# Optimization experiments

Hardware: AMD Instinct MI355X
Metric: run time of the kernel (lower is better)

The kernel has to match this reference:

```python
import jax, jax.numpy as jnp
import numpy as np

NEG_BIG = -9.0e15  # matches torch's -9000000000000000.0 mask fill
ALPHA = 0.2        # leakyrelu negative slope


def setup_inputs() -> dict:
    key = jax.random.key(0)
    k1, k2, k3, k4, k5 = jax.random.split(key, 5)
    N, F_in, F_out = 4096, 512, 64
    stdv = 1.0 / np.sqrt(F_out)
    x = jax.random.normal(k1, (N, F_in), dtype=jnp.float32)
    adj = jax.random.randint(k2, (N, N), 0, 2, dtype=jnp.int32)
    W = jax.random.uniform(k3, (F_in, F_out), dtype=jnp.float32, minval=-stdv, maxval=stdv)
    a = jax.random.normal(k4, (2 * F_out, 1), dtype=jnp.float32) * 0.1
    bias = jax.random.uniform(k5, (F_out,), dtype=jnp.float32, minval=-stdv, maxval=stdv)
    return {"x": x, "adj": adj, "W": W, "a": a, "bias": bias}


def _gat_forward(x, adj, W, a, bias):
    N = x.shape[0]
    F_out = W.shape[1]
    h = x @ W  # (N, F)
    a1 = a[:F_out, 0]   # weights hitting the first concat half
    a2 = a[F_out:, 0]   # weights hitting the second concat half
    # First half: row k=i*N+j of the concat holds h_j  ->  e1[j] = h_j . a1
    e1 = h @ a1  # (N,)
    # Second half of this repo's concat is NOT h_i; exact index algebra:
    # second[k=i*N+j, r] = h[(r*N+i)//F, (((r*N+i)%F)*N + j) % F]
    # Since it depends on j only via j % F, build table T[i, t] (t = j % F).
    r = jnp.arange(F_out)[:, None]          # (F, 1)
    i = jnp.arange(N)[None, :]              # (1, N)
    m = r * N + i                           # (F, N)
    p = m // F_out                          # row index into h
    s0 = m % F_out
    t = jnp.arange(F_out)                   # (F,)
    col = (s0[..., None] * N + t) % F_out   # (F, N, F) column index into h
    vals = h[p[..., None], col]             # (F, N, F)
    T = jnp.einsum('r,rit->it', a2, vals)   # (N, F)
    j = jnp.arange(N)
    e2 = T[:, j % F_out]                    # (N, N) second-half contribution
    e = e1[None, :] + e2                    # (N, N) pre-activation scores
    e = jnp.where(e > 0, e, ALPHA * e)      # LeakyReLU(0.2)
    e = jnp.where(adj > 0, e, NEG_BIG)      # mask non-edges
    att = jax.nn.softmax(e, axis=1)         # row-wise softmax (dropout = eval identity)
    out = jax.nn.relu(att @ h) + bias       # relu BEFORE bias add, as in source
    return out


def reference(x, adj, W, a, bias):
    return _gat_forward(x, adj, W, a, bias)
```

## Files before the change

kernel.cpp:

```cpp
#include <hip/hip_runtime.h>
#include <math.h>

#define N_NODES 4096
#define F_IN    512
#define F_OUT   64
#define ALPHA   0.2f
#define NPART   32

typedef _Float16 half8 __attribute__((ext_vector_type(8)));
typedef _Float16 half4 __attribute__((ext_vector_type(4)));
typedef float    floatx4 __attribute__((ext_vector_type(4)));

__global__ __launch_bounds__(256) void k_prep(const float* __restrict__ W,
                                              _Float16* __restrict__ WT) {
    int idx = blockIdx.x * 256 + threadIdx.x;
    int t = idx >> 9;
    int k = idx & 511;
    WT[idx] = (_Float16)W[k * F_OUT + t];
}

__global__ __launch_bounds__(256) void k_hW(const float* __restrict__ x,
                                            const _Float16* __restrict__ WT,
                                            const float* __restrict__ a,
                                            float* __restrict__ h,
                                            _Float16* __restrict__ hT,
                                            float* __restrict__ e1) {
    __shared__ float red[4][16][64];
    int tid  = threadIdx.x;
    int lane = tid & 63;
    int w    = tid >> 6;
    int i0   = blockIdx.x * 16;
    int n    = lane & 15;
    int quad = lane >> 4;

    floatx4 acc[4] = {{0,0,0,0},{0,0,0,0},{0,0,0,0},{0,0,0,0}};

    const float* xr = x + (size_t)(i0 + n) * F_IN + w * 128 + quad * 8;
    const _Float16* wb = WT + w * 128 + quad * 8;
#pragma unroll
    for (int kk = 0; kk < 128; kk += 32) {
        float4 x0 = *(const float4*)(xr + kk);
        float4 x1 = *(const float4*)(xr + kk + 4);
        half8 af = {(_Float16)x0.x, (_Float16)x0.y, (_Float16)x0.z, (_Float16)x0.w,
                    (_Float16)x1.x, (_Float16)x1.y, (_Float16)x1.z, (_Float16)x1.w};
#pragma unroll
        for (int g = 0; g < 4; ++g) {
            half8 bf = *(const half8*)(wb + (size_t)(g * 16 + n) * F_IN + kk);
            acc[g] = __builtin_amdgcn_mfma_f32_16x16x32_f16(af, bf, acc[g], 0, 0, 0);
        }
    }
#pragma unroll
    for (int g = 0; g < 4; ++g)
#pragma unroll
        for (int r = 0; r < 4; ++r)
            red[w][g * 4 + r][lane] = acc[g][r];
    __syncthreads();
    if (w != 0) return;
#pragma unroll
    for (int g = 0; g < 4; ++g)
#pragma unroll
        for (int r = 0; r < 4; ++r)
            acc[g][r] = red[0][g * 4 + r][lane] + red[1][g * 4 + r][lane] +
                        red[2][g * 4 + r][lane] + red[3][g * 4 + r][lane];
#pragma unroll
    for (int g = 0; g < 4; ++g) {
        half4 hv;
#pragma unroll
        for (int r = 0; r < 4; ++r) {
            h[(size_t)(i0 + quad * 4 + r) * F_OUT + g * 16 + n] = acc[g][r];
            hv[r] = (_Float16)acc[g][r];
        }
        *(half4*)(hT + (size_t)(g * 16 + n) * N_NODES + i0 + quad * 4) = hv;
    }
    float a1v[4];
#pragma unroll
    for (int g = 0; g < 4; ++g) a1v[g] = a[g * 16 + n];
#pragma unroll
    for (int r = 0; r < 4; ++r) {
        float v = acc[0][r] * a1v[0] + acc[1][r] * a1v[1] + acc[2][r] * a1v[2] + acc[3][r] * a1v[3];
        v += __shfl_xor(v, 1, 64);
        v += __shfl_xor(v, 2, 64);
        v += __shfl_xor(v, 4, 64);
        v += __shfl_xor(v, 8, 64);
        if (n == 0) e1[i0 + quad * 4 + r] = v;
    }
}

__global__ __launch_bounds__(256) void k_TqP(const float* __restrict__ h,
                                             const float* __restrict__ a,
                                             const float* __restrict__ e1,
                                             _Float16* __restrict__ P) {
    __shared__ float part[4][64];
    __shared__ float TqS[64];
    int q = blockIdx.x;
    int tid = threadIdx.x;
    int t = tid & 63;
    int rp = tid >> 6;
    const float* a2 = a + F_OUT;
    float s = 0.f;
#pragma unroll
    for (int rr = 0; rr < 16; ++rr) {
        int r = rp * 16 + rr;
        s += a2[r] * h[(size_t)(r * 64 + q) * F_OUT + t];
    }
    part[rp][t] = s;
    __syncthreads();
    if (tid < 64) TqS[tid] = part[0][tid] + part[1][tid] + part[2][tid] + part[3][tid];
    __syncthreads();
#pragma unroll
    for (int it = 0; it < 4; ++it) {
        int j = (it * 256 + tid) * 4;
        float4 ev = *(const float4*)(e1 + j);
        float4 tv = *(const float4*)(TqS + (j & 63));
        float e[4] = {ev.x + tv.x, ev.y + tv.y, ev.z + tv.z, ev.w + tv.w};
        half4 pv;
#pragma unroll
        for (int r = 0; r < 4; ++r) {
            float xx = e[r] > 0.f ? e[r] : ALPHA * e[r];
            pv[r] = (_Float16)__expf(xx);
        }
        *(half4*)(P + (size_t)q * N_NODES + j) = pv;
    }
}

__global__ __launch_bounds__(256, 4) void k_main(const int* __restrict__ adj,
                                                 const _Float16* __restrict__ P,
                                                 const _Float16* __restrict__ hT,
                                                 float* __restrict__ out_part,
                                                 float* __restrict__ den_part) {
    int tid  = threadIdx.x;
    int lane = tid & 63;
    int w    = tid >> 6;
    int b    = blockIdx.x;
    int s    = b & 31;
    int g    = (b >> 5) * 4 + w;
    int i0   = g * 16;
    int q    = i0 >> 6;
    int n    = lane & 15;
    int quad = lane >> 4;
    int jbase = s * 128 + quad * 8;

    const int*      arow = adj + (size_t)(i0 + n) * N_NODES + jbase;
    const _Float16* prow = P + (size_t)q * N_NODES + jbase;
    const _Float16* hrow = hT + (size_t)n * N_NODES + jbase;

    int4 a0[4], a1[4];
    half8 pv[4];
#pragma unroll
    for (int c = 0; c < 4; ++c) {
        a0[c] = *(const int4*)(arow + c * 32);
        a1[c] = *(const int4*)(arow + c * 32 + 4);
        pv[c] = *(const half8*)(prow + c * 32);
    }

    floatx4 acc[4] = {{0,0,0,0},{0,0,0,0},{0,0,0,0},{0,0,0,0}};
    floatx4 accd = {0, 0, 0, 0};
    _Float16 one_h = (n == 0) ? (_Float16)1.0f : (_Float16)0.0f;
    half8 ones_f = {one_h, one_h, one_h, one_h, one_h, one_h, one_h, one_h};

#pragma unroll
    for (int c = 0; c < 4; ++c) {
        int joff = c * 32;
        half8 af;
        af[0] = a0[c].x > 0 ? pv[c][0] : (_Float16)0.f;
        af[1] = a0[c].y > 0 ? pv[c][1] : (_Float16)0.f;
        af[2] = a0[c].z > 0 ? pv[c][2] : (_Float16)0.f;
        af[3] = a0[c].w > 0 ? pv[c][3] : (_Float16)0.f;
        af[4] = a1[c].x > 0 ? pv[c][4] : (_Float16)0.f;
        af[5] = a1[c].y > 0 ? pv[c][5] : (_Float16)0.f;
        af[6] = a1[c].z > 0 ? pv[c][6] : (_Float16)0.f;
        af[7] = a1[c].w > 0 ? pv[c][7] : (_Float16)0.f;
#pragma unroll
        for (int g4 = 0; g4 < 4; ++g4) {
            half8 bf = *(const half8*)(hrow + (size_t)g4 * 16 * N_NODES + joff);
            acc[g4] = __builtin_amdgcn_mfma_f32_16x16x32_f16(af, bf, acc[g4], 0, 0, 0);
        }
        accd = __builtin_amdgcn_mfma_f32_16x16x32_f16(af, ones_f, accd, 0, 0, 0);
    }
    float* op = out_part + ((size_t)s * N_NODES + i0) * F_OUT;
#pragma unroll
    for (int g4 = 0; g4 < 4; ++g4)
#pragma unroll
        for (int r = 0; r < 4; ++r)
            op[(quad * 4 + r) * F_OUT + g4 * 16 + n] = acc[g4][r];
    if (n == 0) {
#pragma unroll
        for (int r = 0; r < 4; ++r)
            den_part[s * N_NODES + i0 + quad * 4 + r] = accd[r];
    }
}

__global__ __launch_bounds__(256) void k_out(const float* __restrict__ out_part,
                                             const float* __restrict__ den_part,
                                             const float* __restrict__ bias,
                                             float* __restrict__ out) {
    int idx4 = blockIdx.x * 256 + threadIdx.x;
    int base = idx4 * 4;
    int i = base >> 6;
    int t = base & 63;
    float4 sacc = {0.f, 0.f, 0.f, 0.f};
    float dacc = 0.f;
#pragma unroll
    for (int p = 0; p < NPART; ++p) {
        float4 v = ((const float4*)(out_part + (size_t)p * N_NODES * F_OUT))[idx4];
        sacc.x += v.x; sacc.y += v.y; sacc.z += v.z; sacc.w += v.w;
        dacc += den_part[p * N_NODES + i];
    }
    float4 bv = *(const float4*)(bias + t);
    float4 o;
    o.x = fmaxf(sacc.x / dacc, 0.f) + bv.x;
    o.y = fmaxf(sacc.y / dacc, 0.f) + bv.y;
    o.z = fmaxf(sacc.z / dacc, 0.f) + bv.z;
    o.w = fmaxf(sacc.w / dacc, 0.f) + bv.w;
    ((float4*)out)[idx4] = o;
}

extern "C" void kernel_launch(void* const* d_in, const int* in_sizes, int n_in,
                              void* d_out, int out_size, void* d_ws, size_t ws_size,
                              hipStream_t stream) {
    const float* x    = (const float*)d_in[0];
    const int*   adj  = (const int*)d_in[1];
    const float* W    = (const float*)d_in[2];
    const float* a    = (const float*)d_in[3];
    const float* bias = (const float*)d_in[4];
    float* out = (float*)d_out;

    char* ws = (char*)d_ws;
    float*    h        = (float*)ws;
    _Float16* hT       = (_Float16*)(ws + 1024 * 1024);
    float*    e1       = (float*)(ws + 1536 * 1024);
    _Float16* P        = (_Float16*)(ws + 1552 * 1024);
    _Float16* WT       = (_Float16*)(ws + 2064 * 1024);
    float*    out_part = (float*)(ws + 2128 * 1024);
    float*    den_part = (float*)(ws + (2128 + 32768) * 1024);

    k_prep<<<128, 256, 0, stream>>>(W, WT);
    k_hW  <<<256, 256, 0, stream>>>(x, WT, a, h, hT, e1);
    k_TqP <<<64, 256, 0, stream>>>(h, a, e1, P);
    k_main<<<2048, 256, 0, stream>>>(adj, P, hT, out_part, den_part);
    k_out <<<256, 256, 0, stream>>>(out_part, den_part, bias, out);
}
```

Baseline: 139.7 us.

## Pack adjacency into bitmask and halve column partitions in main kernel

Adds a kernel that converts the int32 adjacency into a bitmask using wave ballots. The main attention kernel then reads 32-bit mask words and applies them with bitwise AND on the packed half probabilities. The number of column partitions drops from 32 to 16, so each block processes 256 columns, which halves the partial-output buffers and the reduction traffic. The full adjacency is still read once, now coalesced in the pack kernel, at the cost of an extra launch and a mask write.

```diff
diff --git a/kernel.cpp b/kernel.cpp
--- a/kernel.cpp
+++ b/kernel.cpp
@@ -5,11 +5,13 @@
 #define F_IN    512
 #define F_OUT   64
 #define ALPHA   0.2f
-#define NPART   32
+#define NPART   16
 
 typedef _Float16 half8 __attribute__((ext_vector_type(8)));
 typedef _Float16 half4 __attribute__((ext_vector_type(4)));
 typedef float    floatx4 __attribute__((ext_vector_type(4)));
+
+union H8U4 { half8 h; uint32_t u[4]; };
 
 __global__ __launch_bounds__(256) void k_prep(const float* __restrict__ W,
                                               _Float16* __restrict__ WT) {
@@ -17,6 +19,23 @@
     int t = idx >> 9;
     int k = idx & 511;
     WT[idx] = (_Float16)W[k * F_OUT + t];
+}
+
+__global__ __launch_bounds__(256) void k_pack(const int* __restrict__ adj,
+                                              unsigned long long* __restrict__ adjb) {
+    int tid  = threadIdx.x;
+    int lane = tid & 63;
+    int waveId = blockIdx.x * 4 + (tid >> 6);
+    int row  = waveId >> 1;
+    int half = waveId & 1;
+    const int* base = adj + (size_t)row * N_NODES + half * 2048 + lane;
+    unsigned long long* dst = adjb + row * 64 + half * 32;
+#pragma unroll 8
+    for (int c = 0; c < 32; ++c) {
+        int av = base[c * 64];
+        unsigned long long mk = __ballot(av > 0);
+        if (lane == 0) dst[c] = mk;
+    }
 }
 
 __global__ __launch_bounds__(256) void k_hW(const float* __restrict__ x,
@@ -123,7 +142,7 @@
     }
 }
 
-__global__ __launch_bounds__(256, 4) void k_main(const int* __restrict__ adj,
+__global__ __launch_bounds__(256, 4) void k_main(const unsigned int* __restrict__ adjb32,
                                                  const _Float16* __restrict__ P,
                                                  const _Float16* __restrict__ hT,
                                                  float* __restrict__ out_part,
@@ -132,26 +151,21 @@
     int lane = tid & 63;
     int w    = tid >> 6;
     int b    = blockIdx.x;
-    int s    = b & 31;
-    int g    = (b >> 5) * 4 + w;
+    int s    = b & 15;
+    int g    = (b >> 4) * 4 + w;
     int i0   = g * 16;
     int q    = i0 >> 6;
     int n    = lane & 15;
     int quad = lane >> 4;
-    int jbase = s * 128 + quad * 8;
-
-    const int*      arow = adj + (size_t)(i0 + n) * N_NODES + jbase;
+    int jbase = s * 256 + quad * 8;
+
+    const unsigned int* mrow = adjb32 + (size_t)(i0 + n) * (N_NODES / 32) + s * 8;
+    uint4 m0 = *(const uint4*)(mrow);
+    uint4 m1 = *(const uint4*)(mrow + 4);
+    unsigned int m32[8] = {m0.x, m0.y, m0.z, m0.w, m1.x, m1.y, m1.z, m1.w};
+
     const _Float16* prow = P + (size_t)q * N_NODES + jbase;
     const _Float16* hrow = hT + (size_t)n * N_NODES + jbase;
-
-    int4 a0[4], a1[4];
-    half8 pv[4];
-#pragma unroll
-    for (int c = 0; c < 4; ++c) {
-        a0[c] = *(const int4*)(arow + c * 32);
-        a1[c] = *(const int4*)(arow + c * 32 + 4);
-        pv[c] = *(const half8*)(prow + c * 32);
-    }
 
     floatx4 acc[4] = {{0,0,0,0},{0,0,0,0},{0,0,0,0},{0,0,0,0}};
     floatx4 accd = {0, 0, 0, 0};
@@ -159,23 +173,23 @@
     half8 ones_f = {one_h, one_h, one_h, one_h, one_h, one_h, one_h, one_h};
 
 #pragma unroll
-    for (int c = 0; c < 4; ++c) {
+    for (int c = 0; c < 8; ++c) {
         int joff = c * 32;
-        half8 af;
-        af[0] = a0[c].x > 0 ? pv[c][0] : (_Float16)0.f;
-        af[1] = a0[c].y > 0 ? pv[c][1] : (_Float16)0.f;
-        af[2] = a0[c].z > 0 ? pv[c][2] : (_Float16)0.f;
-        af[3] = a0[c].w > 0 ? pv[c][3] : (_Float16)0.f;
-        af[4] = a1[c].x > 0 ? pv[c][4] : (_Float16)0.f;
-        af[5] = a1[c].y > 0 ? pv[c][5] : (_Float16)0.f;
-        af[6] = a1[c].z > 0 ? pv[c][6] : (_Float16)0.f;
-        af[7] = a1[c].w > 0 ? pv[c][7] : (_Float16)0.f;
+        H8U4 pv, af;
+        pv.h = *(const half8*)(prow + joff);
+        unsigned int byte = (m32[c] >> (quad * 8)) & 0xFFu;
+#pragma unroll
+        for (int d = 0; d < 4; ++d) {
+            unsigned int msk = (((byte >> (2 * d)) & 1u) ? 0x0000FFFFu : 0u) |
+                               (((byte >> (2 * d + 1)) & 1u) ? 0xFFFF0000u : 0u);
+            af.u[d] = pv.u[d] & msk;
+        }
 #pragma unroll
         for (int g4 = 0; g4 < 4; ++g4) {
             half8 bf = *(const half8*)(hrow + (size_t)g4 * 16 * N_NODES + joff);
-            acc[g4] = __builtin_amdgcn_mfma_f32_16x16x32_f16(af, bf, acc[g4], 0, 0, 0);
-        }
-        accd = __builtin_amdgcn_mfma_f32_16x16x32_f16(af, ones_f, accd, 0, 0, 0);
+            acc[g4] = __builtin_amdgcn_mfma_f32_16x16x32_f16(af.h, bf, acc[g4], 0, 0, 0);
+        }
+        accd = __builtin_amdgcn_mfma_f32_16x16x32_f16(af.h, ones_f, accd, 0, 0, 0);
     }
     float* op = out_part + ((size_t)s * N_NODES + i0) * F_OUT;
 #pragma unroll
@@ -232,11 +246,13 @@
     _Float16* P        = (_Float16*)(ws + 1552 * 1024);
     _Float16* WT       = (_Float16*)(ws + 2064 * 1024);
     float*    out_part = (float*)(ws + 2128 * 1024);
-    float*    den_part = (float*)(ws + (2128 + 32768) * 1024);
+    float*    den_part = (float*)(ws + (2128 + 16384) * 1024);
+    unsigned long long* adjb = (unsigned long long*)(ws + (2128 + 16384 + 256) * 1024);
 
     k_prep<<<128, 256, 0, stream>>>(W, WT);
+    k_pack<<<2048, 256, 0, stream>>>(adj, adjb);
     k_hW  <<<256, 256, 0, stream>>>(x, WT, a, h, hT, e1);
     k_TqP <<<64, 256, 0, stream>>>(h, a, e1, P);
-    k_main<<<2048, 256, 0, stream>>>(adj, P, hT, out_part, den_part);
+    k_main<<<1024, 256, 0, stream>>>((const unsigned int*)adjb, P, hT, out_part, den_part);
     k_out <<<256, 256, 0, stream>>>(out_part, den_part, bias, out);
 }
```

Result: slower. 151.8 us (+8.7%).

## Stage adj, hT and P tiles via async global-to-LDS loads in k_main

Applied to the files above, without the earlier changes.

k_main now copies its adjacency, hT and P tiles into shared memory with global_load_lds, instead of loading them directly into registers. The hT slice is now shared across the four waves rather than each wave loading all of it. Masking is done with bitwise AND on packed half pairs instead of per-element selects. k_TqP is split into four blocks per q to raise parallelism. In exchange, k_main uses about 41KB of LDS, lowers its occupancy hint from 4 to 3, and adds a block barrier before compute.

```diff
diff --git a/kernel.cpp b/kernel.cpp
--- a/kernel.cpp
+++ b/kernel.cpp
@@ -10,6 +10,14 @@
 typedef _Float16 half8 __attribute__((ext_vector_type(8)));
 typedef _Float16 half4 __attribute__((ext_vector_type(4)));
 typedef float    floatx4 __attribute__((ext_vector_type(4)));
+
+union H8U4 { half8 h; uint32_t u[4]; };
+
+__device__ __forceinline__ void async_copy16(void* lds, const void* g) {
+    __builtin_amdgcn_global_load_lds(
+        (const __attribute__((address_space(1))) unsigned int*)g,
+        (__attribute__((address_space(3))) unsigned int*)lds, 16, 0, 0);
+}
 
 __global__ __launch_bounds__(256) void k_prep(const float* __restrict__ W,
                                               _Float16* __restrict__ WT) {
@@ -92,7 +100,9 @@
                                              _Float16* __restrict__ P) {
     __shared__ float part[4][64];
     __shared__ float TqS[64];
-    int q = blockIdx.x;
+    int b = blockIdx.x;
+    int q = b >> 2;
+    int quarter = b & 3;
     int tid = threadIdx.x;
     int t = tid & 63;
     int rp = tid >> 6;
@@ -107,51 +117,51 @@
     __syncthreads();
     if (tid < 64) TqS[tid] = part[0][tid] + part[1][tid] + part[2][tid] + part[3][tid];
     __syncthreads();
-#pragma unroll
-    for (int it = 0; it < 4; ++it) {
-        int j = (it * 256 + tid) * 4;
-        float4 ev = *(const float4*)(e1 + j);
-        float4 tv = *(const float4*)(TqS + (j & 63));
-        float e[4] = {ev.x + tv.x, ev.y + tv.y, ev.z + tv.z, ev.w + tv.w};
-        half4 pv;
-#pragma unroll
-        for (int r = 0; r < 4; ++r) {
-            float xx = e[r] > 0.f ? e[r] : ALPHA * e[r];
-            pv[r] = (_Float16)__expf(xx);
-        }
-        *(half4*)(P + (size_t)q * N_NODES + j) = pv;
-    }
-}
-
-__global__ __launch_bounds__(256, 4) void k_main(const int* __restrict__ adj,
+    int j = quarter * 1024 + tid * 4;
+    float4 ev = *(const float4*)(e1 + j);
+    float4 tv = *(const float4*)(TqS + (j & 63));
+    float e[4] = {ev.x + tv.x, ev.y + tv.y, ev.z + tv.z, ev.w + tv.w};
+    half4 pv;
+#pragma unroll
+    for (int r = 0; r < 4; ++r) {
+        float xx = e[r] > 0.f ? e[r] : ALPHA * e[r];
+        pv[r] = (_Float16)__expf(xx);
+    }
+    *(half4*)(P + (size_t)q * N_NODES + j) = pv;
+}
+
+__global__ __launch_bounds__(256, 3) void k_main(const int* __restrict__ adj,
                                                  const _Float16* __restrict__ P,
                                                  const _Float16* __restrict__ hT,
                                                  float* __restrict__ out_part,
                                                  float* __restrict__ den_part) {
+    __shared__ int      lds_adj[4][8][256];
+    __shared__ _Float16 lds_B[16][512];
+    __shared__ _Float16 lds_P[512];
+
     int tid  = threadIdx.x;
     int lane = tid & 63;
     int w    = tid >> 6;
     int b    = blockIdx.x;
+    int rb   = b >> 5;
     int s    = b & 31;
-    int g    = (b >> 5) * 4 + w;
-    int i0   = g * 16;
-    int q    = i0 >> 6;
+    int i0   = rb * 64 + w * 16;
     int n    = lane & 15;
     int quad = lane >> 4;
-    int jbase = s * 128 + quad * 8;
-
-    const int*      arow = adj + (size_t)(i0 + n) * N_NODES + jbase;
-    const _Float16* prow = P + (size_t)q * N_NODES + jbase;
-    const _Float16* hrow = hT + (size_t)n * N_NODES + jbase;
-
-    int4 a0[4], a1[4];
-    half8 pv[4];
+
+    const int* adj_base = adj + (size_t)(i0 + n) * N_NODES + s * 128 + quad * 8;
 #pragma unroll
     for (int c = 0; c < 4; ++c) {
-        a0[c] = *(const int4*)(arow + c * 32);
-        a1[c] = *(const int4*)(arow + c * 32 + 4);
-        pv[c] = *(const half8*)(prow + c * 32);
-    }
+        async_copy16(&lds_adj[w][c * 2 + 0][0], adj_base + c * 32);
+        async_copy16(&lds_adj[w][c * 2 + 1][0], adj_base + c * 32 + 4);
+    }
+    const _Float16* hT_base = hT + (size_t)(w * 16 + n) * N_NODES + s * 128 + quad * 8;
+#pragma unroll
+    for (int c = 0; c < 4; ++c)
+        async_copy16(&lds_B[w * 4 + c][0], hT_base + c * 32);
+    if (w == 0)
+        async_copy16(&lds_P[0], P + (size_t)rb * N_NODES + s * 128 + lane * 8);
+    __syncthreads();
 
     floatx4 acc[4] = {{0,0,0,0},{0,0,0,0},{0,0,0,0},{0,0,0,0}};
     floatx4 accd = {0, 0, 0, 0};
@@ -160,23 +170,22 @@
 
 #pragma unroll
     for (int c = 0; c < 4; ++c) {
-        int joff = c * 32;
-        half8 af;
-        af[0] = a0[c].x > 0 ? pv[c][0] : (_Float16)0.f;
-        af[1] = a0[c].y > 0 ? pv[c][1] : (_Float16)0.f;
-        af[2] = a0[c].z > 0 ? pv[c][2] : (_Float16)0.f;
-        af[3] = a0[c].w > 0 ? pv[c][3] : (_Float16)0.f;
-        af[4] = a1[c].x > 0 ? pv[c][4] : (_Float16)0.f;
-        af[5] = a1[c].y > 0 ? pv[c][5] : (_Float16)0.f;
-        af[6] = a1[c].z > 0 ? pv[c][6] : (_Float16)0.f;
-        af[7] = a1[c].w > 0 ? pv[c][7] : (_Float16)0.f;
+        int4 ga = *(const int4*)&lds_adj[w][c * 2 + 0][lane * 4];
+        int4 gb = *(const int4*)&lds_adj[w][c * 2 + 1][lane * 4];
+        H8U4 pv, af;
+        pv.h = *(const half8*)&lds_P[c * 32 + quad * 8];
+        af.u[0] = pv.u[0] & ((ga.x > 0 ? 0x0000FFFFu : 0u) | (ga.y > 0 ? 0xFFFF0000u : 0u));
+        af.u[1] = pv.u[1] & ((ga.z > 0 ? 0x0000FFFFu : 0u) | (ga.w > 0 ? 0xFFFF0000u : 0u));
+        af.u[2] = pv.u[2] & ((gb.x > 0 ? 0x0000FFFFu : 0u) | (gb.y > 0 ? 0xFFFF0000u : 0u));
+        af.u[3] = pv.u[3] & ((gb.z > 0 ? 0x0000FFFFu : 0u) | (gb.w > 0 ? 0xFFFF0000u : 0u));
 #pragma unroll
         for (int g4 = 0; g4 < 4; ++g4) {
-            half8 bf = *(const half8*)(hrow + (size_t)g4 * 16 * N_NODES + joff);
-            acc[g4] = __builtin_amdgcn_mfma_f32_16x16x32_f16(af, bf, acc[g4], 0, 0, 0);
+            half8 bf = *(const half8*)&lds_B[g4 * 4 + c][lane * 8];
+            acc[g4] = __builtin_amdgcn_mfma_f32_16x16x32_f16(af.h, bf, acc[g4], 0, 0, 0);
         }
-        accd = __builtin_amdgcn_mfma_f32_16x16x32_f16(af, ones_f, accd, 0, 0, 0);
-    }
+        accd = __builtin_amdgcn_mfma_f32_16x16x32_f16(af.h, ones_f, accd, 0, 0, 0);
+    }
+
     float* op = out_part + ((size_t)s * N_NODES + i0) * F_OUT;
 #pragma unroll
     for (int g4 = 0; g4 < 4; ++g4)
@@ -236,7 +245,7 @@
 
     k_prep<<<128, 256, 0, stream>>>(W, WT);
     k_hW  <<<256, 256, 0, stream>>>(x, WT, a, h, hT, e1);
-    k_TqP <<<64, 256, 0, stream>>>(h, a, e1, P);
+    k_TqP <<<256, 256, 0, stream>>>(h, a, e1, P);
     k_main<<<2048, 256, 0, stream>>>(adj, P, hT, out_part, den_part);
     k_out <<<256, 256, 0, stream>>>(out_part, den_part, bias, out);
 }
```

Result: faster. 128.6 us (-7.9%).
